# Kernel tuning notes

Hardware: AMD Instinct MI355X
Metric: run time of the kernel (lower is better)

The kernel has to match this reference:

```python
import jax, jax.numpy as jnp
import numpy as np

S = 512  # number of sampled points (init kwarg s)


def farthest_point_sample(xyz, s):
    """Iterative FPS. xyz: [B, N, 3] -> idx: [B, s] int32.
    Deterministic start at index 0 (torch reference uses a random start)."""
    B, N, _ = xyz.shape

    def step(carry, _):
        dist, farthest = carry  # dist: [B, N], farthest: [B]
        centroid = jnp.take_along_axis(xyz, farthest[:, None, None], axis=1)  # [B,1,3]
        d = jnp.sum((xyz - centroid) ** 2, axis=-1)  # [B, N]
        dist = jnp.minimum(dist, d)
        nxt = jnp.argmax(dist, axis=-1).astype(jnp.int32)  # [B]
        return (dist, nxt), farthest

    init = (jnp.full((B, N), 1e10, dtype=xyz.dtype), jnp.zeros((B,), dtype=jnp.int32))
    _, idx = jax.lax.scan(step, init, None, length=s)  # idx: [s, B]
    return idx.T  # [B, s]


def index_points(points, idx):
    """points: [B, N, C], idx: [B, s] -> [B, s, C]."""
    return jnp.take_along_axis(points, idx[:, :, None], axis=1)


def setup_inputs() -> dict:
    key = jax.random.key(0)
    k1, k2 = jax.random.split(key)
    B, N, C = 32, 65536, 64
    xyz = jax.random.normal(k1, (B, N, 3), dtype=jnp.float32)
    f = jax.random.normal(k2, (B, N, C), dtype=jnp.float32)
    return {"xyz": xyz, "f": f}


def reference(xyz, f):
    idx = farthest_point_sample(xyz, S)
    xyz_sampled = index_points(xyz, idx)
    f_sampled = index_points(f, idx)
    return (xyz_sampled, f_sampled)
```

## Files before the change

### kernel.cpp

```cpp
#include <hip/hip_runtime.h>


#define BATCH 32
#define NPTS  65536
#define NSAMP 512
#define NCH   64
#define NBLK_PER_B 8
#define TPB   512
#define CHUNK (NPTS / NBLK_PER_B)
#define PPT   (CHUNK / TPB)
#define NWAVE (TPB / 64)

__global__ __launch_bounds__(TPB, 1) void fps_kernel(
    const float* __restrict__ xyz,
    unsigned long long* __restrict__ slots,
    int* __restrict__ winners)
{
    const int bx    = blockIdx.x;
    const int b     = bx & (BATCH - 1);
    const int chunk = bx >> 5;
    const int tid   = threadIdx.x;
    const float* xb = xyz + (size_t)b * NPTS * 3;
    const int base  = chunk * CHUNK;

    float px[PPT], py[PPT], pz[PPT], dist[PPT];
#pragma unroll
    for (int i = 0; i < PPT; ++i) {
        int n = base + i * TPB + tid;
        const float* p = xb + (size_t)n * 3;
        px[i] = p[0]; py[i] = p[1]; pz[i] = p[2];
        dist[i] = 1e10f;
    }

    __shared__ float red_v[NWAVE];
    __shared__ int   red_n[NWAVE];
    __shared__ float cxyz[3];

    unsigned long long* slot_b = slots + (size_t)b * NSAMP * NBLK_PER_B;
    int* win_b = winners + b * NSAMP;

    float cx = xb[0], cy = xb[1], cz = xb[2];

    for (int s = 0; s < NSAMP - 1; ++s) {
        float bv = -1.0f;
        int   bn = 0;
#pragma unroll
        for (int i = 0; i < PPT; ++i) {
            float dx = px[i] - cx;
            float dy = py[i] - cy;
            float dz = pz[i] - cz;
            float d  = __fadd_rn(__fadd_rn(__fmul_rn(dx, dx), __fmul_rn(dy, dy)),
                                 __fmul_rn(dz, dz));
            float nd = fminf(dist[i], d);
            dist[i] = nd;
            if (nd > bv) { bv = nd; bn = base + i * TPB + tid; }
        }
#pragma unroll
        for (int off = 32; off >= 1; off >>= 1) {
            float pv = __shfl_down(bv, off, 64);
            int   pn = __shfl_down(bn, off, 64);
            if (pv > bv || (pv == bv && pn < bn)) { bv = pv; bn = pn; }
        }
        if ((tid & 63) == 0) { red_v[tid >> 6] = bv; red_n[tid >> 6] = bn; }
        __syncthreads();

        if (tid < 64) {
            float fv = (tid < NWAVE) ? red_v[tid] : -1.0f;
            int   fn = (tid < NWAVE) ? red_n[tid] : 0x7fffffff;
#pragma unroll
            for (int off = 4; off >= 1; off >>= 1) {
                float pv = __shfl_xor(fv, off, 64);
                int   pn = __shfl_xor(fn, off, 64);
                if (pv > fv || (pv == fv && pn < fn)) { fv = pv; fn = pn; }
            }
            unsigned long long* line = slot_b + (size_t)s * NBLK_PER_B;
            if (tid == 0) {
                unsigned long long packed =
                    ((unsigned long long)__float_as_uint(fv) << 32) |
                    (unsigned int)(~fn);
                __hip_atomic_store(&line[chunk], packed,
                                   __ATOMIC_RELAXED, __HIP_MEMORY_SCOPE_AGENT);
            }
            const int li = (tid < NBLK_PER_B) ? tid : (NBLK_PER_B - 1);
            unsigned long long v;
            for (;;) {
                v = __hip_atomic_load(&line[li], __ATOMIC_RELAXED,
                                      __HIP_MEMORY_SCOPE_AGENT);
                if (__all(v != 0)) break;
                __builtin_amdgcn_s_sleep(1);
            }
#pragma unroll
            for (int off = 4; off >= 1; off >>= 1) {
                unsigned long long pv = __shfl_xor(v, off, 64);
                if (pv > v) v = pv;
            }
            if (tid == 0) {
                int far = (int)(~(unsigned int)v);
                if (chunk == 0) win_b[s] = far;
                const float* cp = xb + (size_t)far * 3;
                cxyz[0] = cp[0]; cxyz[1] = cp[1]; cxyz[2] = cp[2];
            }
        }
        __syncthreads();
        cx = cxyz[0]; cy = cxyz[1]; cz = cxyz[2];
    }
}

__global__ __launch_bounds__(256) void gather_kernel(
    const float* __restrict__ xyz,
    const float* __restrict__ f,
    const int* __restrict__ winners,
    float* __restrict__ out_xyz,
    float* __restrict__ out_f)
{
    const int t  = threadIdx.x;
    const int g  = blockIdx.x * 4 + (t >> 6);
    const int ln = t & 63;
    const int b  = g >> 9;
    const int s  = g & (NSAMP - 1);

    int n = (s == 0) ? 0 : winners[b * NSAMP + (s - 1)];

    out_f[((size_t)b * NSAMP + s) * NCH + ln] = f[((size_t)b * NPTS + n) * NCH + ln];
    if (ln < 3)
        out_xyz[((size_t)b * NSAMP + s) * 3 + ln] =
            xyz[((size_t)b * NPTS + n) * 3 + ln];
}

extern "C" void kernel_launch(void* const* d_in, const int* in_sizes, int n_in,
                              void* d_out, int out_size, void* d_ws, size_t ws_size,
                              hipStream_t stream) {
    const float* xyz = (const float*)d_in[0];
    const float* f   = (const float*)d_in[1];
    float* out_xyz = (float*)d_out;
    float* out_f   = (float*)d_out + (size_t)BATCH * NSAMP * 3;

    unsigned long long* slots = (unsigned long long*)d_ws;
    int* winners = (int*)((char*)d_ws +
                          (size_t)BATCH * NSAMP * NBLK_PER_B * 8);

    hipMemsetAsync(d_ws, 0, (size_t)BATCH * NSAMP * NBLK_PER_B * 8, stream);

    fps_kernel<<<BATCH * NBLK_PER_B, TPB, 0, stream>>>(xyz, slots, winners);
    gather_kernel<<<BATCH * NSAMP / 4, 256, 0, stream>>>(xyz, f, winners,
                                                         out_xyz, out_f);
}
```

Baseline: 1.741 ms.

## Publish winner centroid in tagged double-buffered slots and poll from all waves

The cross-block FPS reduction moves from per-sample zero-initialised atomic slots to two reusable 64-byte lines per block, selected by the parity of the iteration. Each line carries the packed max key, a per-iteration tag and the winning point's coordinates. Every wave now polls these lines with inline-asm cache-control loads and derives the next centroid directly, which removes the dependent global load of the winner's coordinates and the second block barrier. The 16-bit index packing relies on NPTS fitting in 16 bits. Safety rests on the tag and double-buffer protocol and on hand-written cache-bit stores, which makes it fragile.

```diff
diff --git a/kernel.cpp b/kernel.cpp
--- a/kernel.cpp
+++ b/kernel.cpp
@@ -5,21 +5,56 @@
 #define NPTS  65536
 #define NSAMP 512
 #define NCH   64
-#define NBLK_PER_B 8
+#define NBLK  8
 #define TPB   512
-#define CHUNK (NPTS / NBLK_PER_B)
+#define CHUNK (NPTS / NBLK)
 #define PPT   (CHUNK / TPB)
 #define NWAVE (TPB / 64)
+#define NITER (NSAMP - 1)
+#define POLL_CAP 512
+
+typedef unsigned int       u32;
+typedef unsigned long long u64;
+typedef __attribute__((ext_vector_type(4))) u32 u32x4;
+typedef __attribute__((ext_vector_type(2))) u32 u32x2;
+
+#define LINES_BYTES (BATCH * 2 * NBLK * 64)
+
+__device__ __forceinline__ void slot_publish(u64 addr, u32x4 a, u32x2 b) {
+    asm volatile(
+        "global_store_dwordx4 %0, %1, off sc0 sc1\n\t"
+        "global_store_dwordx2 %0, %2, off offset:16 sc0 sc1\n\t"
+        "global_store_dwordx4 %0, %1, off sc0\n\t"
+        "global_store_dwordx2 %0, %2, off offset:16 sc0"
+        :: "v"(addr), "v"(a), "v"(b) : "memory");
+}
+
+__device__ __forceinline__ void slot_load(u64 addr, u32x4& a, u32x2& b,
+                                          bool fast) {
+    if (fast)
+        asm volatile(
+            "global_load_dwordx4 %0, %2, off sc0\n\t"
+            "global_load_dwordx2 %1, %2, off offset:16 sc0\n\t"
+            "s_waitcnt vmcnt(0)"
+            : "=&v"(a), "=&v"(b) : "v"(addr) : "memory");
+    else
+        asm volatile(
+            "global_load_dwordx4 %0, %2, off sc0 sc1\n\t"
+            "global_load_dwordx2 %1, %2, off offset:16 sc0 sc1\n\t"
+            "s_waitcnt vmcnt(0)"
+            : "=&v"(a), "=&v"(b) : "v"(addr) : "memory");
+}
 
 __global__ __launch_bounds__(TPB, 1) void fps_kernel(
     const float* __restrict__ xyz,
-    unsigned long long* __restrict__ slots,
+    char* __restrict__ ws,
     int* __restrict__ winners)
 {
     const int bx    = blockIdx.x;
     const int b     = bx & (BATCH - 1);
     const int chunk = bx >> 5;
     const int tid   = threadIdx.x;
+    const int lane  = tid & 63;
     const float* xb = xyz + (size_t)b * NPTS * 3;
     const int base  = chunk * CHUNK;
 
@@ -32,16 +67,17 @@
         dist[i] = 1e10f;
     }
 
-    __shared__ float red_v[NWAVE];
-    __shared__ int   red_n[NWAVE];
-    __shared__ float cxyz[3];
+    __shared__ u64 red[2][NWAVE];
 
-    unsigned long long* slot_b = slots + (size_t)b * NSAMP * NBLK_PER_B;
+    const u64 lines_b = (u64)(ws) + (u64)b * (2 * NBLK * 64);
     int* win_b = winners + b * NSAMP;
 
     float cx = xb[0], cy = xb[1], cz = xb[2];
+    bool fast = true;
 
-    for (int s = 0; s < NSAMP - 1; ++s) {
+    for (int s = 0; s < NITER; ++s) {
+        const u32 tag = (u32)(s + 1);
+
         float bv = -1.0f;
         int   bn = 0;
 #pragma unroll
@@ -55,54 +91,60 @@
             dist[i] = nd;
             if (nd > bv) { bv = nd; bn = base + i * TPB + tid; }
         }
+
+        u64 pk = ((u64)__float_as_uint(bv) << 32)
+               | (u64)((tag << 16) | (u32)(0xFFFF ^ bn));
 #pragma unroll
         for (int off = 32; off >= 1; off >>= 1) {
-            float pv = __shfl_down(bv, off, 64);
-            int   pn = __shfl_down(bn, off, 64);
-            if (pv > bv || (pv == bv && pn < bn)) { bv = pv; bn = pn; }
+            u64 o = __shfl_down(pk, off, 64);
+            if (o > pk) pk = o;
         }
-        if ((tid & 63) == 0) { red_v[tid >> 6] = bv; red_n[tid >> 6] = bn; }
+        if (lane == 0) red[s & 1][tid >> 6] = pk;
         __syncthreads();
 
+        const u64 line = lines_b + (u64)((s & 1) * (NBLK * 64));
+
         if (tid < 64) {
-            float fv = (tid < NWAVE) ? red_v[tid] : -1.0f;
-            int   fn = (tid < NWAVE) ? red_n[tid] : 0x7fffffff;
+            u64 bpk = red[s & 1][lane & 7];
 #pragma unroll
             for (int off = 4; off >= 1; off >>= 1) {
-                float pv = __shfl_xor(fv, off, 64);
-                int   pn = __shfl_xor(fn, off, 64);
-                if (pv > fv || (pv == fv && pn < fn)) { fv = pv; fn = pn; }
-            }
-            unsigned long long* line = slot_b + (size_t)s * NBLK_PER_B;
-            if (tid == 0) {
-                unsigned long long packed =
-                    ((unsigned long long)__float_as_uint(fv) << 32) |
-                    (unsigned int)(~fn);
-                __hip_atomic_store(&line[chunk], packed,
-                                   __ATOMIC_RELAXED, __HIP_MEMORY_SCOPE_AGENT);
-            }
-            const int li = (tid < NBLK_PER_B) ? tid : (NBLK_PER_B - 1);
-            unsigned long long v;
-            for (;;) {
-                v = __hip_atomic_load(&line[li], __ATOMIC_RELAXED,
-                                      __HIP_MEMORY_SCOPE_AGENT);
-                if (__all(v != 0)) break;
-                __builtin_amdgcn_s_sleep(1);
-            }
-#pragma unroll
-            for (int off = 4; off >= 1; off >>= 1) {
-                unsigned long long pv = __shfl_xor(v, off, 64);
-                if (pv > v) v = pv;
+                u64 o = __shfl_xor(bpk, off, 64);
+                if (o > bpk) bpk = o;
             }
             if (tid == 0) {
-                int far = (int)(~(unsigned int)v);
-                if (chunk == 0) win_b[s] = far;
-                const float* cp = xb + (size_t)far * 3;
-                cxyz[0] = cp[0]; cxyz[1] = cp[1]; cxyz[2] = cp[2];
+                int n = 0xFFFF ^ (u32)(bpk & 0xFFFF);
+                const float* cp = xb + (size_t)n * 3;
+                u32x4 a; u32x2 bb;
+                a.x = (u32)bpk;            a.y = (u32)(bpk >> 32);
+                a.z = __float_as_uint(cp[0]); a.w = __float_as_uint(cp[1]);
+                bb.x = __float_as_uint(cp[2]); bb.y = tag;
+                slot_publish(line + (u64)chunk * 64, a, bb);
             }
         }
-        __syncthreads();
-        cx = cxyz[0]; cy = cxyz[1]; cz = cxyz[2];
+
+        u32x4 A; u32x2 Bv;
+        const u64 myaddr = line + (u64)((lane & 7) * 64);
+        int tries = 0;
+        for (;;) {
+            slot_load(myaddr, A, Bv, fast);
+            if (__all(((A.x >> 16) == tag) && (Bv.y == tag))) break;
+            if (++tries >= POLL_CAP) fast = false;
+            __builtin_amdgcn_s_sleep(1);
+        }
+
+        u64 pkw = ((u64)A.y << 32) | A.x;
+        u64 m = pkw;
+#pragma unroll
+        for (int off = 4; off >= 1; off >>= 1) {
+            u64 o = __shfl_xor(m, off, 64);
+            if (o > m) m = o;
+        }
+        int wl = __ffsll((u64)(__ballot(pkw == m) & 0xFFull)) - 1;
+        cx = __uint_as_float(__shfl(A.z, wl, 64));
+        cy = __uint_as_float(__shfl(A.w, wl, 64));
+        cz = __uint_as_float(__shfl(Bv.x, wl, 64));
+        if (chunk == 0 && tid == 0)
+            win_b[s] = 0xFFFF ^ (u32)(m & 0xFFFF);
     }
 }
 
@@ -135,13 +177,12 @@
     float* out_xyz = (float*)d_out;
     float* out_f   = (float*)d_out + (size_t)BATCH * NSAMP * 3;
 
-    unsigned long long* slots = (unsigned long long*)d_ws;
-    int* winners = (int*)((char*)d_ws +
-                          (size_t)BATCH * NSAMP * NBLK_PER_B * 8);
+    char* ws      = (char*)d_ws;
+    int*  winners = (int*)((char*)d_ws + LINES_BYTES);
 
-    hipMemsetAsync(d_ws, 0, (size_t)BATCH * NSAMP * NBLK_PER_B * 8, stream);
+    hipMemsetAsync(d_ws, 0, LINES_BYTES, stream);
 
-    fps_kernel<<<BATCH * NBLK_PER_B, TPB, 0, stream>>>(xyz, slots, winners);
+    fps_kernel<<<BATCH * NBLK, TPB, 0, stream>>>(xyz, ws, winners);
     gather_kernel<<<BATCH * NSAMP / 4, 256, 0, stream>>>(xyz, f, winners,
                                                          out_xyz, out_f);
 }
```

New measurement: 2.545 ms. 1.46x slower.
